# Performance work log

Measured on AMD Instinct MI355X. Metric: run time of the kernel, lower is better.

## Reference

```python
import jax, jax.numpy as jnp
import numpy as np

PAD = 1
K = 3  # kernel_size


def conv2d(x, w, b):
    y = jax.lax.conv_general_dilated(
        x, w, window_strides=(1, 1), padding=((PAD, PAD), (PAD, PAD)),
        dimension_numbers=("NCHW", "OIHW", "NCHW"))
    return y + b[None, :, None, None]


def deform_conv2d(x, offset, weight, bias):
    # torchvision.ops.deform_conv2d semantics (stride=1, dilation=1, 1 offset group)
    B, C, H, W = x.shape
    O = weight.shape[0]
    K2 = K * K
    off = offset.reshape(B, K2, 2, H, W)  # [...,0]=dy, [...,1]=dx
    ky, kx = jnp.meshgrid(jnp.arange(K), jnp.arange(K), indexing="ij")
    ky = ky.reshape(K2).astype(x.dtype)
    kx = kx.reshape(K2).astype(x.dtype)
    hh = jnp.arange(H, dtype=x.dtype)
    ww = jnp.arange(W, dtype=x.dtype)
    # sampling coords, shape [B, K2, H, W]
    py = off[:, :, 0] + ky[None, :, None, None] + hh[None, None, :, None] - PAD
    px = off[:, :, 1] + kx[None, :, None, None] + ww[None, None, None, :] - PAD

    y0 = jnp.floor(py)
    x0 = jnp.floor(px)
    wy = (py - y0)[:, None]  # [B,1,K2,H,W]
    wx = (px - x0)[:, None]

    xf = x.reshape(B, C, H * W)

    def gather(iy, ix):
        valid = (iy >= 0) & (iy < H) & (ix >= 0) & (ix < W)
        iyc = jnp.clip(iy, 0, H - 1).astype(jnp.int32)
        ixc = jnp.clip(ix, 0, W - 1).astype(jnp.int32)
        idx = (iyc * W + ixc).reshape(B, 1, K2 * H * W)
        v = jnp.take_along_axis(xf, idx, axis=2).reshape(B, C, K2, H, W)
        return v * valid.reshape(B, 1, K2, H, W).astype(x.dtype)

    v00 = gather(y0, x0)
    v01 = gather(y0, x0 + 1)
    v10 = gather(y0 + 1, x0)
    v11 = gather(y0 + 1, x0 + 1)
    sampled = (v00 * (1 - wy) * (1 - wx) + v01 * (1 - wy) * wx
               + v10 * wy * (1 - wx) + v11 * wy * wx)  # [B,C,K2,H,W]
    out = jnp.einsum("bckhw,ock->bohw", sampled, weight.reshape(O, C, K2))
    return out + bias[None, :, None, None]


def setup_inputs() -> dict:
    key = jax.random.key(0)
    k1, k2, k3, k4, k5 = jax.random.split(key, 5)
    B, C, H, W = 4, 64, 192, 192
    O = 64
    x = jax.random.normal(k1, (B, C, H, W), dtype=jnp.float32)
    w_off = jax.random.normal(k2, (2 * K * K, C, K, K), dtype=jnp.float32) * 0.05
    b_off = jnp.zeros((2 * K * K,), dtype=jnp.float32)
    w_conv = jax.random.normal(k3, (O, C, K, K), dtype=jnp.float32) * (1.0 / np.sqrt(C * K * K))
    b_conv = jax.random.normal(k4, (O,), dtype=jnp.float32) * 0.01
    return {"x": x, "w_off": w_off, "b_off": b_off, "w_conv": w_conv, "b_conv": b_conv}


def reference(x, w_off, b_off, w_conv, b_conv):
    offset = conv2d(x, w_off, b_off)
    y = deform_conv2d(x, offset, w_conv, b_conv)
    return conv2d(y, w_conv, b_conv)  # module reuses self.conv on deform output
```

## Files before the change

kernel.cpp:

```cpp
#include <hip/hip_runtime.h>

constexpr int B = 4;
constexpr int C = 64;
constexpr int O = 64;
constexpr int OOFF = 18;
constexpr int H = 192;
constexpr int W = 192;

typedef __attribute__((ext_vector_type(8))) short short8;
typedef __attribute__((ext_vector_type(4))) float float4v;
typedef __attribute__((ext_vector_type(2))) float f32x2;
typedef __attribute__((ext_vector_type(2))) uint u32x2;
typedef __attribute__((ext_vector_type(2))) __bf16 bf16x2;

__device__ inline ushort f2bf(float f) {
  return __builtin_bit_cast(ushort, (__bf16)f);
}
__device__ inline uint pk2bf(float lo, float hi) {
  bf16x2 v;
  v.x = (__bf16)lo;
  v.y = (__bf16)hi;
  return __builtin_bit_cast(uint, v);
}
__device__ inline f32x2 upk(uint u) {
  u32x2 t;
  t.x = u << 16;
  t.y = u & 0xffff0000u;
  return __builtin_bit_cast(f32x2, t);
}

__global__ __launch_bounds__(256) void k_pre(const float* __restrict__ x,
                                             ushort* __restrict__ xtb,
                                             const float* __restrict__ w_conv,
                                             ushort* __restrict__ wBf,
                                             const float* __restrict__ w_off,
                                             ushort* __restrict__ wOf) {
  __shared__ float tile[64][17];
  const int bid = blockIdx.x;
  const int tid = threadIdx.x;
  if (bid < 9216) {
    const int w0 = (bid % 12) * 16;
    const int h = (bid / 12) % 192;
    const int b = bid / 2304;
    const int wl = tid & 15;
    const int c0 = tid >> 4;
#pragma unroll
    for (int r = 0; r < 4; ++r) {
      const int c = c0 + r * 16;
      tile[c][wl] = x[(((size_t)b * C + c) * H + h) * W + w0 + wl];
    }
    __syncthreads();
    const int c = tid & 63;
    const int qq = tid >> 6;
#pragma unroll
    for (int r = 0; r < 4; ++r) {
      const int wq = qq + r * 4;
      xtb[(((size_t)b * H + h) * W + w0 + wq) * C + c] = f2bf(tile[c][wq]);
    }
  } else if (bid < 9360) {
    const int i = (bid - 9216) * 256 + tid;
    const int j = i & 7;
    const int lane = (i >> 3) & 63;
    const int nt = (i >> 9) & 3;
    const int kstep = (i >> 11) & 1;
    const int kk = i >> 12;
    const int n = nt + 4 * (lane & 15);
    const int c = kstep * 32 + ((lane >> 4) & 3) * 8 + j;
    wBf[i] = f2bf(w_conv[((size_t)n * C + c) * 9 + kk]);
  } else {
    const int i = (bid - 9360) * 256 + tid;
    const int j = i & 7;
    const int lane = (i >> 3) & 63;
    const int nt = (i >> 9) & 1;
    const int ks = (i >> 10) & 1;
    const int kk = i >> 11;
    const int n = nt * 16 + (lane & 15);
    const int c = ks * 32 + ((lane >> 4) & 3) * 8 + j;
    wOf[i] = (n < OOFF) ? f2bf(w_off[((size_t)n * C + c) * 9 + kk]) : (ushort)0;
  }
}

__global__ __launch_bounds__(256) void k_fused(
    const ushort* __restrict__ xtb, const ushort* __restrict__ wOf,
    const float* __restrict__ b_off, const ushort* __restrict__ wBf,
    const float* __restrict__ b_conv, ushort* __restrict__ yt) {
  __shared__ ushort sA[4][2][64][8];
  __shared__ __align__(16) float offBuf[4][16][20];

  const int bid = blockIdx.x;
  const int xcd = bid & 7;
  const int s0 = bid >> 3;
  const int b = xcd >> 1;
  const int half = xcd & 1;
  const int th = half * 12 + s0 / 24;
  const int tw = s0 % 24;
  const int h0 = th * 8, w0 = tw * 8;

  const int tid = threadIdx.x;
  const int wave = tid >> 6, lane = tid & 63;
  const int col = lane & 15, quad = lane >> 4;
  const int p = tid >> 2, qtr = tid & 3;
  const int pl = p & 15;
  const int prow = p >> 3, pcol = p & 7;
  const int h = h0 + prow, w = w0 + pcol;
  const int ks_w = qtr >> 1;
  const int q2 = (qtr & 1) * 2;

  {
    float4v oacc[2];
#pragma unroll
    for (int nt = 0; nt < 2; ++nt) oacc[nt] = (float4v){0.f, 0.f, 0.f, 0.f};

    short8 oafr[2][2];

    auto oload = [&](int kk, int pb) {
      const int ky = kk / 3, kx = kk % 3;
      const int hh = h0 + 2 * wave + (col >> 3) + ky - 1;
      const int ww = w0 + (col & 7) + kx - 1;
      const bool ok = ((unsigned)hh < (unsigned)H) && ((unsigned)ww < (unsigned)W);
      const int hhc = min(max(hh, 0), H - 1);
      const int wwc = min(max(ww, 0), W - 1);
      const ushort* pa = xtb + (((size_t)b * H + hhc) * W + wwc) * C + quad * 8;
#pragma unroll
      for (int ks = 0; ks < 2; ++ks) {
        short8 v = (short8)0;
        if (ok) v = *(const short8*)(pa + ks * 32);
        oafr[pb][ks] = v;
      }
    };

    oload(0, 0);
#pragma unroll
    for (int kk = 0; kk < 9; ++kk) {
      const int pb = kk & 1;
      if (kk < 8) oload(kk + 1, pb ^ 1);
#pragma unroll
      for (int ks = 0; ks < 2; ++ks)
#pragma unroll
        for (int nt = 0; nt < 2; ++nt) {
          const short8 bw =
              *(const short8*)&wOf[((((size_t)kk * 2 + ks) * 2 + nt) * 64 + lane) * 8];
          oacc[nt] = __builtin_amdgcn_mfma_f32_16x16x32_bf16(oafr[pb][ks], bw, oacc[nt], 0, 0, 0);
        }
    }

#pragma unroll
    for (int nt = 0; nt < 2; ++nt) {
      const int oc = nt * 16 + col;
      if (oc < OOFF) {
        const float bias = b_off[oc];
#pragma unroll
        for (int r = 0; r < 4; ++r)
          offBuf[wave][quad * 4 + r][oc] = oacc[nt][r] + bias;
      }
    }
  }

  const ushort* xbase = xtb + (size_t)b * H * W * C;
  const uint qoff = (uint)qtr * 32u;

  uint offs[2][4];
  float4 awv[2];
  uint4 gA[4], gB[4];

  auto calc = [&](int kk, int s) {
    const float2 ov = *(const float2*)&offBuf[wave][pl][2 * kk];
    const float dy = ov.x, dx = ov.y;
    const int ky = kk / 3, kx = kk % 3;
    const float pyf = dy + (float)(ky + h - 1);
    const float pxf = dx + (float)(kx + w - 1);
    const float fy0 = floorf(pyf), fx0 = floorf(pxf);
    const float wy = pyf - fy0, wx = pxf - fx0;
    const int iy0 = (int)fy0, ix0 = (int)fx0;
    const int iy1 = iy0 + 1, ix1 = ix0 + 1;
    const bool vy0 = (unsigned)iy0 < (unsigned)H;
    const bool vy1 = (unsigned)iy1 < (unsigned)H;
    const bool vx0 = (unsigned)ix0 < (unsigned)W;
    const bool vx1 = (unsigned)ix1 < (unsigned)W;
    awv[s].x = (vy0 && vx0) ? (1.f - wy) * (1.f - wx) : 0.f;
    awv[s].y = (vy0 && vx1) ? (1.f - wy) * wx : 0.f;
    awv[s].z = (vy1 && vx0) ? wy * (1.f - wx) : 0.f;
    awv[s].w = (vy1 && vx1) ? wy * wx : 0.f;
    const int cy0 = min(max(iy0, 0), H - 1), cy1 = min(max(iy1, 0), H - 1);
    const int cx0 = min(max(ix0, 0), W - 1), cx1 = min(max(ix1, 0), W - 1);
    offs[s][0] = (uint)((cy0 * W + cx0) * (C * 2)) + qoff;
    offs[s][1] = (uint)((cy0 * W + cx1) * (C * 2)) + qoff;
    offs[s][2] = (uint)((cy1 * W + cx0) * (C * 2)) + qoff;
    offs[s][3] = (uint)((cy1 * W + cx1) * (C * 2)) + qoff;
  };

  auto loadA = [&](int s) {
#pragma unroll
    for (int c = 0; c < 4; ++c)
      gA[c] = *(const uint4*)((const char*)xbase + offs[s][c]);
  };
  auto loadB = [&](int s) {
#pragma unroll
    for (int c = 0; c < 4; ++c)
      gB[c] = *(const uint4*)((const char*)xbase + offs[s][c] + 16u);
  };
  auto blend = [&](const uint4* g, int s, uint* pk) {
    const f32x2 a00 = {awv[s].x, awv[s].x};
    const f32x2 a01 = {awv[s].y, awv[s].y};
    const f32x2 a10 = {awv[s].z, awv[s].z};
    const f32x2 a11 = {awv[s].w, awv[s].w};
#pragma unroll
    for (int i = 0; i < 4; ++i) {
      f32x2 sv = upk(g[0][i]) * a00 + upk(g[1][i]) * a01 + upk(g[2][i]) * a10 + upk(g[3][i]) * a11;
      pk[i] = pk2bf(sv.x, sv.y);
    }
  };

  float4v acc[4];
#pragma unroll
  for (int nt = 0; nt < 4; ++nt) acc[nt] = (float4v){0.f, 0.f, 0.f, 0.f};

  calc(0, 0);
  loadA(0);
#pragma unroll
  for (int kk = 0; kk < 9; ++kk) {
    const int s = kk & 1, ns = s ^ 1;
    loadB(s);
    if (kk < 8) calc(kk + 1, ns);

    uint pkA[4];
    blend(gA, s, pkA);
    *(uint4*)&sA[wave][ks_w][pl | (q2 << 4)][0] = *(const uint4*)pkA;
    if (kk < 8) loadA(ns);

    uint pkB[4];
    blend(gB, s, pkB);
    *(uint4*)&sA[wave][ks_w][pl | ((q2 + 1) << 4)][0] = *(const uint4*)pkB;

#pragma unroll
    for (int ks = 0; ks < 2; ++ks) {
      const short8 a = *(const short8*)&sA[wave][ks][lane][0];
#pragma unroll
      for (int nt = 0; nt < 4; ++nt) {
        const short8 bb = *(const short8*)&wBf[((((size_t)kk * 2 + ks) * 4 + nt) * 64 + lane) * 8];
        acc[nt] = __builtin_amdgcn_mfma_f32_16x16x32_bf16(a, bb, acc[nt], 0, 0, 0);
      }
    }
  }

  float bias[4];
#pragma unroll
  for (int nt = 0; nt < 4; ++nt) bias[nt] = b_conv[4 * col + nt];
#pragma unroll
  for (int r = 0; r < 4; ++r) {
    const int pp = wave * 16 + quad * 4 + r;
    const int hrow = h0 + (pp >> 3), wcol = w0 + (pp & 7);
    uint2 u;
    u.x = pk2bf(acc[0][r] + bias[0], acc[1][r] + bias[1]);
    u.y = pk2bf(acc[2][r] + bias[2], acc[3][r] + bias[3]);
    *(uint2*)&yt[((size_t)(b * H + hrow) * W + wcol) * C + 4 * col] = u;
  }
}

__global__ __launch_bounds__(256) void k_conv_main_mfma(
    const ushort* __restrict__ yt, const ushort* __restrict__ wBf,
    const float* __restrict__ b_conv, float* __restrict__ out) {
  const int w0 = blockIdx.x * 16;
  const int b = blockIdx.z;
  const int tid = threadIdx.x;
  const int wave = tid >> 6, lane = tid & 63;
  const int col = lane & 15, quad = lane >> 4;
  const int h0 = blockIdx.y * 8 + wave * 2;

  float4v acc[2][4];
#pragma unroll
  for (int mt = 0; mt < 2; ++mt)
#pragma unroll
    for (int nt = 0; nt < 4; ++nt) acc[mt][nt] = (float4v){0.f, 0.f, 0.f, 0.f};

  short8 bfr[2][2][4];
  short8 afr[2][2][2];

  auto load = [&](int kk, int pb) {
    const int ky = kk / 3, kx = kk % 3;
    const int ww = w0 + col + kx - 1;
    const bool wok = (unsigned)ww < (unsigned)W;
    const int wwc = min(max(ww, 0), W - 1);
#pragma unroll
    for (int ks = 0; ks < 2; ++ks)
#pragma unroll
      for (int nt = 0; nt < 4; ++nt)
        bfr[pb][ks][nt] = *(const short8*)&wBf[((((size_t)kk * 2 + ks) * 4 + nt) * 64 + lane) * 8];
#pragma unroll
    for (int mt = 0; mt < 2; ++mt) {
      const int hh = h0 + mt + ky - 1;
      const bool ok = wok && ((unsigned)hh < (unsigned)H);
      const int hhc = min(max(hh, 0), H - 1);
      const ushort* pa = yt + (((size_t)b * H + hhc) * W + wwc) * C + quad * 8;
#pragma unroll
      for (int ks = 0; ks < 2; ++ks) {
        short8 v = (short8)0;
        if (ok) v = *(const short8*)(pa + ks * 32);
        afr[pb][mt][ks] = v;
      }
    }
  };

  load(0, 0);
#pragma unroll
  for (int kk = 0; kk < 9; ++kk) {
    const int pb = kk & 1;
    if (kk < 8) load(kk + 1, pb ^ 1);
#pragma unroll
    for (int ks = 0; ks < 2; ++ks)
#pragma unroll
      for (int mt = 0; mt < 2; ++mt)
#pragma unroll
        for (int nt = 0; nt < 4; ++nt)
          acc[mt][nt] = __builtin_amdgcn_mfma_f32_16x16x32_bf16(afr[pb][mt][ks], bfr[pb][ks][nt],
                                                                acc[mt][nt], 0, 0, 0);
  }

  float bias[4];
#pragma unroll
  for (int nt = 0; nt < 4; ++nt) bias[nt] = b_conv[4 * col + nt];
#pragma unroll
  for (int mt = 0; mt < 2; ++mt) {
    const int h = h0 + mt;
#pragma unroll
    for (int nt = 0; nt < 4; ++nt) {
      const int oc = 4 * col + nt;
      float4 v;
      v.x = acc[mt][nt][0] + bias[nt];
      v.y = acc[mt][nt][1] + bias[nt];
      v.z = acc[mt][nt][2] + bias[nt];
      v.w = acc[mt][nt][3] + bias[nt];
      *(float4*)&out[(((size_t)b * O + oc) * H + h) * W + w0 + quad * 4] = v;
    }
  }
}

extern "C" void kernel_launch(void* const* d_in, const int* in_sizes, int n_in,
                              void* d_out, int out_size, void* d_ws, size_t ws_size,
                              hipStream_t stream) {
  const float* x = (const float*)d_in[0];
  const float* w_off = (const float*)d_in[1];
  const float* b_off = (const float*)d_in[2];
  const float* w_conv = (const float*)d_in[3];
  const float* b_conv = (const float*)d_in[4];
  float* out = (float*)d_out;

  ushort* xtb = (ushort*)d_ws;
  ushort* yt = xtb + (size_t)B * H * W * C;
  ushort* wBf = yt + (size_t)B * H * W * C;
  ushort* wOf = wBf + 36864;

  const dim3 blk(256);
  k_pre<<<dim3(9432), blk, 0, stream>>>(x, xtb, w_conv, wBf, w_off, wOf);
  k_fused<<<dim3(2304), blk, 0, stream>>>(xtb, wOf, b_off, wBf, b_conv, yt);
  k_conv_main_mfma<<<dim3(W / 16, H / 8, B), blk, 0, stream>>>(yt, wBf, b_conv, out);
}
```

Baseline: 199.3 us.

## Halve block sizes and drop register double-buffering in fused and conv kernels

Both the fused deformable kernel and the final conv kernel move from 256-thread to 128-thread blocks, with twice as many blocks. The fused kernel drops its two-stage software pipeline of offsets and weights, loading both halves of each bilinear sample after the blend instead. The final conv kernel processes one row per wave instead of two and reads weights inline instead of double-buffering them. The goal is lower register pressure and higher occupancy, at the cost of less latency hiding inside each wave and less reuse of weight fragments across rows.

```diff
diff --git a/kernel.cpp b/kernel.cpp
--- a/kernel.cpp
+++ b/kernel.cpp
@@ -80,27 +80,28 @@
   }
 }
 
-__global__ __launch_bounds__(256) void k_fused(
+__global__ __launch_bounds__(128) void k_fused(
     const ushort* __restrict__ xtb, const ushort* __restrict__ wOf,
     const float* __restrict__ b_off, const ushort* __restrict__ wBf,
     const float* __restrict__ b_conv, ushort* __restrict__ yt) {
-  __shared__ ushort sA[4][2][64][8];
-  __shared__ __align__(16) float offBuf[4][16][20];
+  __shared__ ushort sA[2][2][64][8];
+  __shared__ __align__(16) float offBuf[2][16][20];
 
   const int bid = blockIdx.x;
   const int xcd = bid & 7;
   const int s0 = bid >> 3;
   const int b = xcd >> 1;
   const int half = xcd & 1;
-  const int th = half * 12 + s0 / 24;
+  const int th = s0 / 24;
   const int tw = s0 % 24;
-  const int h0 = th * 8, w0 = tw * 8;
 
   const int tid = threadIdx.x;
   const int wave = tid >> 6, lane = tid & 63;
+  const int h0 = half * 96 + th * 4 + wave * 2;
+  const int w0 = tw * 8;
+
   const int col = lane & 15, quad = lane >> 4;
-  const int p = tid >> 2, qtr = tid & 3;
-  const int pl = p & 15;
+  const int p = lane >> 2, qtr = lane & 3;
   const int prow = p >> 3, pcol = p & 7;
   const int h = h0 + prow, w = w0 + pcol;
   const int ks_w = qtr >> 1;
@@ -115,7 +116,7 @@
 
     auto oload = [&](int kk, int pb) {
       const int ky = kk / 3, kx = kk % 3;
-      const int hh = h0 + 2 * wave + (col >> 3) + ky - 1;
+      const int hh = h0 + (col >> 3) + ky - 1;
       const int ww = w0 + (col & 7) + kx - 1;
       const bool ok = ((unsigned)hh < (unsigned)H) && ((unsigned)ww < (unsigned)W);
       const int hhc = min(max(hh, 0), H - 1);
@@ -158,17 +159,17 @@
 
   const ushort* xbase = xtb + (size_t)b * H * W * C;
   const uint qoff = (uint)qtr * 32u;
-
-  uint offs[2][4];
-  float4 awv[2];
+  const float hm1 = (float)(h - 1), wm1 = (float)(w - 1);
+
+  uint offs[4];
+  float4 awv;
   uint4 gA[4], gB[4];
 
-  auto calc = [&](int kk, int s) {
-    const float2 ov = *(const float2*)&offBuf[wave][pl][2 * kk];
-    const float dy = ov.x, dx = ov.y;
+  auto calc = [&](int kk) {
+    const float2 ov = *(const float2*)&offBuf[wave][p][2 * kk];
     const int ky = kk / 3, kx = kk % 3;
-    const float pyf = dy + (float)(ky + h - 1);
-    const float pxf = dx + (float)(kx + w - 1);
+    const float pyf = ov.x + hm1 + (float)ky;
+    const float pxf = ov.y + wm1 + (float)kx;
     const float fy0 = floorf(pyf), fx0 = floorf(pxf);
     const float wy = pyf - fy0, wx = pxf - fx0;
     const int iy0 = (int)fy0, ix0 = (int)fx0;
@@ -177,33 +178,31 @@
     const bool vy1 = (unsigned)iy1 < (unsigned)H;
     const bool vx0 = (unsigned)ix0 < (unsigned)W;
     const bool vx1 = (unsigned)ix1 < (unsigned)W;
-    awv[s].x = (vy0 && vx0) ? (1.f - wy) * (1.f - wx) : 0.f;
-    awv[s].y = (vy0 && vx1) ? (1.f - wy) * wx : 0.f;
-    awv[s].z = (vy1 && vx0) ? wy * (1.f - wx) : 0.f;
-    awv[s].w = (vy1 && vx1) ? wy * wx : 0.f;
+    awv.x = (vy0 && vx0) ? (1.f - wy) * (1.f - wx) : 0.f;
+    awv.y = (vy0 && vx1) ? (1.f - wy) * wx : 0.f;
+    awv.z = (vy1 && vx0) ? wy * (1.f - wx) : 0.f;
+    awv.w = (vy1 && vx1) ? wy * wx : 0.f;
     const int cy0 = min(max(iy0, 0), H - 1), cy1 = min(max(iy1, 0), H - 1);
     const int cx0 = min(max(ix0, 0), W - 1), cx1 = min(max(ix1, 0), W - 1);
-    offs[s][0] = (uint)((cy0 * W + cx0) * (C * 2)) + qoff;
-    offs[s][1] = (uint)((cy0 * W + cx1) * (C * 2)) + qoff;
-    offs[s][2] = (uint)((cy1 * W + cx0) * (C * 2)) + qoff;
-    offs[s][3] = (uint)((cy1 * W + cx1) * (C * 2)) + qoff;
+    offs[0] = (uint)((cy0 * W + cx0) * (C * 2)) + qoff;
+    offs[1] = (uint)((cy0 * W + cx1) * (C * 2)) + qoff;
+    offs[2] = (uint)((cy1 * W + cx0) * (C * 2)) + qoff;
+    offs[3] = (uint)((cy1 * W + cx1) * (C * 2)) + qoff;
   };
 
-  auto loadA = [&](int s) {
+  auto loadAB = [&]() {
 #pragma unroll
     for (int c = 0; c < 4; ++c)
-      gA[c] = *(const uint4*)((const char*)xbase + offs[s][c]);
+      gA[c] = *(const uint4*)((const char*)xbase + offs[c]);
+#pragma unroll
+    for (int c = 0; c < 4; ++c)
+      gB[c] = *(const uint4*)((const char*)xbase + offs[c] + 16u);
   };
-  auto loadB = [&](int s) {
-#pragma unroll
-    for (int c = 0; c < 4; ++c)
-      gB[c] = *(const uint4*)((const char*)xbase + offs[s][c] + 16u);
-  };
-  auto blend = [&](const uint4* g, int s, uint* pk) {
-    const f32x2 a00 = {awv[s].x, awv[s].x};
-    const f32x2 a01 = {awv[s].y, awv[s].y};
-    const f32x2 a10 = {awv[s].z, awv[s].z};
-    const f32x2 a11 = {awv[s].w, awv[s].w};
+  auto blend = [&](const uint4* g, uint* pk) {
+    const f32x2 a00 = {awv.x, awv.x};
+    const f32x2 a01 = {awv.y, awv.y};
+    const f32x2 a10 = {awv.z, awv.z};
+    const f32x2 a11 = {awv.w, awv.w};
 #pragma unroll
     for (int i = 0; i < 4; ++i) {
       f32x2 sv = upk(g[0][i]) * a00 + upk(g[1][i]) * a01 + upk(g[2][i]) * a10 + upk(g[3][i]) * a11;
@@ -215,22 +214,21 @@
 #pragma unroll
   for (int nt = 0; nt < 4; ++nt) acc[nt] = (float4v){0.f, 0.f, 0.f, 0.f};
 
-  calc(0, 0);
-  loadA(0);
+  calc(0);
+  loadAB();
 #pragma unroll
   for (int kk = 0; kk < 9; ++kk) {
-    const int s = kk & 1, ns = s ^ 1;
-    loadB(s);
-    if (kk < 8) calc(kk + 1, ns);
-
     uint pkA[4];
-    blend(gA, s, pkA);
-    *(uint4*)&sA[wave][ks_w][pl | (q2 << 4)][0] = *(const uint4*)pkA;
-    if (kk < 8) loadA(ns);
-
+    blend(gA, pkA);
+    *(uint4*)&sA[wave][ks_w][p | (q2 << 4)][0] = *(const uint4*)pkA;
     uint pkB[4];
-    blend(gB, s, pkB);
-    *(uint4*)&sA[wave][ks_w][pl | ((q2 + 1) << 4)][0] = *(const uint4*)pkB;
+    blend(gB, pkB);
+    *(uint4*)&sA[wave][ks_w][p | ((q2 + 1) << 4)][0] = *(const uint4*)pkB;
+
+    if (kk < 8) {
+      calc(kk + 1);
+      loadAB();
+    }
 
 #pragma unroll
     for (int ks = 0; ks < 2; ++ks) {
@@ -248,7 +246,7 @@
   for (int nt = 0; nt < 4; ++nt) bias[nt] = b_conv[4 * col + nt];
 #pragma unroll
   for (int r = 0; r < 4; ++r) {
-    const int pp = wave * 16 + quad * 4 + r;
+    const int pp = quad * 4 + r;
     const int hrow = h0 + (pp >> 3), wcol = w0 + (pp & 7);
     uint2 u;
     u.x = pk2bf(acc[0][r] + bias[0], acc[1][r] + bias[1]);
@@ -257,7 +255,7 @@
   }
 }
 
-__global__ __launch_bounds__(256) void k_conv_main_mfma(
+__global__ __launch_bounds__(128) void k_conv_main_mfma(
     const ushort* __restrict__ yt, const ushort* __restrict__ wBf,
     const float* __restrict__ b_conv, float* __restrict__ out) {
   const int w0 = blockIdx.x * 16;
@@ -265,39 +263,27 @@
   const int tid = threadIdx.x;
   const int wave = tid >> 6, lane = tid & 63;
   const int col = lane & 15, quad = lane >> 4;
-  const int h0 = blockIdx.y * 8 + wave * 2;
-
-  float4v acc[2][4];
-#pragma unroll
-  for (int mt = 0; mt < 2; ++mt)
-#pragma unroll
-    for (int nt = 0; nt < 4; ++nt) acc[mt][nt] = (float4v){0.f, 0.f, 0.f, 0.f};
-
-  short8 bfr[2][2][4];
-  short8 afr[2][2][2];
+  const int h = blockIdx.y * 2 + wave;
+
+  float4v acc[4];
+#pragma unroll
+  for (int nt = 0; nt < 4; ++nt) acc[nt] = (float4v){0.f, 0.f, 0.f, 0.f};
+
+  short8 afr[2][2];
 
   auto load = [&](int kk, int pb) {
     const int ky = kk / 3, kx = kk % 3;
     const int ww = w0 + col + kx - 1;
-    const bool wok = (unsigned)ww < (unsigned)W;
+    const int hh = h + ky - 1;
+    const bool ok = ((unsigned)ww < (unsigned)W) && ((unsigned)hh < (unsigned)H);
     const int wwc = min(max(ww, 0), W - 1);
-#pragma unroll
-    for (int ks = 0; ks < 2; ++ks)
-#pragma unroll
-      for (int nt = 0; nt < 4; ++nt)
-        bfr[pb][ks][nt] = *(const short8*)&wBf[((((size_t)kk * 2 + ks) * 4 + nt) * 64 + lane) * 8];
-#pragma unroll
-    for (int mt = 0; mt < 2; ++mt) {
-      const int hh = h0 + mt + ky - 1;
-      const bool ok = wok && ((unsigned)hh < (unsigned)H);
-      const int hhc = min(max(hh, 0), H - 1);
-      const ushort* pa = yt + (((size_t)b * H + hhc) * W + wwc) * C + quad * 8;
-#pragma unroll
-      for (int ks = 0; ks < 2; ++ks) {
-        short8 v = (short8)0;
-        if (ok) v = *(const short8*)(pa + ks * 32);
-        afr[pb][mt][ks] = v;
-      }
+    const int hhc = min(max(hh, 0), H - 1);
+    const ushort* pa = yt + (((size_t)b * H + hhc) * W + wwc) * C + quad * 8;
+#pragma unroll
+    for (int ks = 0; ks < 2; ++ks) {
+      short8 v = (short8)0;
+      if (ok) v = *(const short8*)(pa + ks * 32);
+      afr[pb][ks] = v;
     }
   };
 
@@ -309,29 +295,24 @@
 #pragma unroll
     for (int ks = 0; ks < 2; ++ks)
 #pragma unroll
-      for (int mt = 0; mt < 2; ++mt)
-#pragma unroll
-        for (int nt = 0; nt < 4; ++nt)
-          acc[mt][nt] = __builtin_amdgcn_mfma_f32_16x16x32_bf16(afr[pb][mt][ks], bfr[pb][ks][nt],
-                                                                acc[mt][nt], 0, 0, 0);
+      for (int nt = 0; nt < 4; ++nt) {
+        const short8 bb = *(const short8*)&wBf[((((size_t)kk * 2 + ks) * 4 + nt) * 64 + lane) * 8];
+        acc[nt] = __builtin_amdgcn_mfma_f32_16x16x32_bf16(afr[pb][ks], bb, acc[nt], 0, 0, 0);
+      }
   }
 
   float bias[4];
 #pragma unroll
   for (int nt = 0; nt < 4; ++nt) bias[nt] = b_conv[4 * col + nt];
 #pragma unroll
-  for (int mt = 0; mt < 2; ++mt) {
-    const int h = h0 + mt;
-#pragma unroll
-    for (int nt = 0; nt < 4; ++nt) {
-      const int oc = 4 * col + nt;
-      float4 v;
-      v.x = acc[mt][nt][0] + bias[nt];
-      v.y = acc[mt][nt][1] + bias[nt];
-      v.z = acc[mt][nt][2] + bias[nt];
-      v.w = acc[mt][nt][3] + bias[nt];
-      *(float4*)&out[(((size_t)b * O + oc) * H + h) * W + w0 + quad * 4] = v;
-    }
+  for (int nt = 0; nt < 4; ++nt) {
+    const int oc = 4 * col + nt;
+    float4 v;
+    v.x = acc[nt][0] + bias[nt];
+    v.y = acc[nt][1] + bias[nt];
+    v.z = acc[nt][2] + bias[nt];
+    v.w = acc[nt][3] + bias[nt];
+    *(float4*)&out[(((size_t)b * O + oc) * H + h) * W + w0 + quad * 4] = v;
   }
 }
 
@@ -350,8 +331,7 @@
   ushort* wBf = yt + (size_t)B * H * W * C;
   ushort* wOf = wBf + 36864;
 
-  const dim3 blk(256);
-  k_pre<<<dim3(9432), blk, 0, stream>>>(x, xtb, w_conv, wBf, w_off, wOf);
-  k_fused<<<dim3(2304), blk, 0, stream>>>(xtb, wOf, b_off, wBf, b_conv, yt);
-  k_conv_main_mfma<<<dim3(W / 16, H / 8, B), blk, 0, stream>>>(yt, wBf, b_conv, out);
-}
+  k_pre<<<dim3(9432), dim3(256), 0, stream>>>(x, xtb, w_conv, wBf, w_off, wOf);
+  k_fused<<<dim3(4608), dim3(128), 0, stream>>>(xtb, wOf, b_off, wBf, b_conv, yt);
+  k_conv_main_mfma<<<dim3(W / 16, H / 2, B), dim3(128), 0, stream>>>(yt, wBf, b_conv, out);
+}
```

Result: slower. 209.2 us (+5.0%).
